# Performance work log

Measured on AMD Instinct MI355X. Metric: run time of the kernel, lower is better.

## Reference

```python
import jax, jax.numpy as jnp
import numpy as np
import math

B, H, S, DK = 2, 16, 2048, 64

def setup_inputs() -> dict:
    key = jax.random.key(0)
    kq, kk, kv, km = jax.random.split(key, 4)
    q = jax.random.normal(kq, (B, H, S, DK), dtype=jnp.float32)
    k = jax.random.normal(kk, (B, H, S, DK), dtype=jnp.float32)
    v = jax.random.normal(kv, (B, H, S, DK), dtype=jnp.float32)
    mask = jax.random.randint(km, (1, 1, S, S), 0, 2).astype(jnp.bool_)
    return {"q": q, "k": k, "v": v, "mask": mask}

def reference(q, k, v, mask):
    d_k = q.shape[-1]
    # scores: [B,H,Sq,Sk]
    scores = jnp.einsum('bhqd,bhkd->bhqk', q, k) / math.sqrt(d_k)
    scores = jnp.where(mask, jnp.float32(-1e9), scores)
    # NOTE: original uses nn.Softmax(dim=2) -> softmax over the QUERY axis
    attn = jax.nn.softmax(scores, axis=2)
    out = jnp.einsum('bhqk,bhkd->bhqd', attn, v)
    return out
```

## Files before the change

### kernel.cpp

```cpp
#include <hip/hip_runtime.h>
#include <math.h>

#define S_LEN 2048
#define NCH   32
#define N_BH  32

typedef short bf16x8 __attribute__((ext_vector_type(8)));
typedef _Float16 f16x8 __attribute__((ext_vector_type(8)));
typedef float f32x4  __attribute__((ext_vector_type(4)));
typedef unsigned short u16;
typedef unsigned short u16x8 __attribute__((ext_vector_type(8)));
typedef unsigned long long u64;

#define MFMA32(a,b,c) __builtin_amdgcn_mfma_f32_16x16x32_bf16((a),(b),(c),0,0,0)
#define MFMAH(a,b,c)  __builtin_amdgcn_mfma_f32_16x16x32_f16((a),(b),(c),0,0,0)
#define EXP2(x) __builtin_amdgcn_exp2f(x)

#define SC        0.18033688011112042f
#define MASKED_L2 (-14.0f)

__device__ __forceinline__ u16 f2h(float x) {
  union { _Float16 h; u16 u; } v;
  v.h = (_Float16)x;
  return v.u;
}
__device__ __forceinline__ u16 f2bf_rne(float x) {
  unsigned u = __float_as_uint(x);
  return (u16)((u + 0x7FFF + ((u >> 16) & 1)) >> 16);
}
__device__ __forceinline__ void bfsplit(float x, u16& h, u16& l) {
  unsigned u = __float_as_uint(x);
  h = (u16)(u >> 16);
  float hf = __uint_as_float(u & 0xFFFF0000u);
  l = f2bf_rne(x - hf);
}

__global__ __launch_bounds__(256) void pack_mask(
    const int* __restrict__ mask, u64* __restrict__ bits) {
  const int word = blockIdx.x * 4 + (threadIdx.x >> 6);
  const int lane = threadIdx.x & 63;
  const int row = word >> 5, wc = word & 31;
  int m = mask[(size_t)row * S_LEN + wc * 64 + lane];
  u64 b = __ballot(m != 0);
  if (lane == 0) bits[word] = b;
}

__global__ __launch_bounds__(256) void prep_qk(
    const float* __restrict__ Q, const float* __restrict__ K,
    u16* __restrict__ qf, u16* __restrict__ kf) {
  const int tid = threadIdx.x;
  const int slot = tid & 15, r0 = tid >> 4;
  const size_t rowbase = (size_t)blockIdx.x * 64;
#pragma unroll
  for (int p = 0; p < 4; ++p) {
    const size_t row = rowbase + p * 16 + r0;
    const size_t dst = row * 64 + ((slot * 4) ^ (((int)row & 7) << 3));
    float4 xq = *(const float4*)(Q + row * 64 + slot * 4);
    *(ushort4*)(qf + dst) = make_ushort4(
        f2h(xq.x * SC), f2h(xq.y * SC), f2h(xq.z * SC), f2h(xq.w * SC));
    float4 xk = *(const float4*)(K + row * 64 + slot * 4);
    *(ushort4*)(kf + dst) = make_ushort4(
        f2h(xk.x), f2h(xk.y), f2h(xk.z), f2h(xk.w));
  }
}

__global__ __launch_bounds__(256) void prep_w(
    const float* __restrict__ V, const float* __restrict__ part,
    u16* __restrict__ w_t) {
  __shared__ __align__(16) u16 ts[4096];
  const int tid = threadIdx.x;
  const int kc = blockIdx.x, bh = blockIdx.y;
  const int k = tid >> 2, dblk = (tid & 3) * 16;
  const size_t ko = (size_t)bh * S_LEN + kc * 64 + k;
  const float lsum = part[ko] + part[65536 + ko]
                   + part[131072 + ko] + part[196608 + ko];
  const float ilk = 1.0f / lsum;
  const float* vb = V + ko * 64 + dblk;
#pragma unroll
  for (int u = 0; u < 4; ++u) {
    float4 x = *(const float4*)(vb + u * 4);
    float xs[4] = {x.x, x.y, x.z, x.w};
#pragma unroll
    for (int e = 0; e < 4; ++e) {
      const int d = dblk + u * 4 + e;
      ts[d * 64 + (k ^ ((d & 7) << 3))] = f2h(xs[e] * ilk);
    }
  }
  __syncthreads();
  u16* dst = w_t + ((size_t)bh * NCH + kc) * 4096;
#pragma unroll
  for (int j = 0; j < 2; ++j)
    *(u16x8*)(dst + j * 2048 + tid * 8) = *(const u16x8*)(ts + j * 2048 + tid * 8);
}

__global__ __launch_bounds__(512, 4) void passA(
    const u16* __restrict__ qf, const u16* __restrict__ kf,
    const u64* __restrict__ mbits, float* __restrict__ part) {
  __shared__ __align__(16) u16 qbuf[4096];

  const int tid = threadIdx.x;
  const int lane = tid & 63;
  const int w = tid >> 6;
  const int c = lane & 15;
  const int g = lane >> 4;
  const int bx = blockIdx.x;
  const int bh = blockIdx.y;
  const int qp = blockIdx.z;

  const size_t bh_off = (size_t)bh * S_LEN * 64;
  const int swc = (c & 7) << 3;

  f16x8 ka[2][2];
#pragma unroll
  for (int t = 0; t < 2; ++t) {
    const int row = bx * 256 + w * 32 + t * 16 + c;
#pragma unroll
    for (int h = 0; h < 2; ++h)
      ka[t][h] = *(const f16x8*)(kf + bh_off + (size_t)row * 64
                                 + ((h * 32 + g * 8) ^ swc));
  }

  u16x8 stg = *(const u16x8*)(qf + bh_off + (size_t)(qp * 512) * 64 + tid * 8);

  float lp[2][4] = {{0.f, 0.f, 0.f, 0.f}, {0.f, 0.f, 0.f, 0.f}};
  const int word = bx * 4 + (w >> 1);
  const int sh0 = (w & 1) * 32;

  for (int qs = 0; qs < 8; ++qs) {
    __syncthreads();
    *(u16x8*)(qbuf + tid * 8) = stg;
    __syncthreads();
    if (qs + 1 < 8)
      stg = *(const u16x8*)(qf + bh_off
            + (size_t)(qp * 512 + (qs + 1) * 64) * 64 + tid * 8);

#pragma unroll
    for (int sub = 0; sub < 4; ++sub) {
      f16x8 fh[2];
      const int rb = sub * 1024 + c * 64;
#pragma unroll
      for (int h = 0; h < 2; ++h)
        fh[h] = *(const f16x8*)(qbuf + rb + ((h * 32 + g * 8) ^ swc));
      const int qrow = qp * 512 + qs * 64 + sub * 16 + c;
      const u64 mw = mbits[(size_t)qrow * NCH + word];
#pragma unroll
      for (int t = 0; t < 2; ++t) {
        f32x4 acc = {0.f, 0.f, 0.f, 0.f};
        acc = MFMAH(ka[t][0], fh[0], acc);
        acc = MFMAH(ka[t][1], fh[1], acc);
        const unsigned nib = (unsigned)(mw >> (sh0 + t * 16 + g * 4)) & 0xFu;
#pragma unroll
        for (int r = 0; r < 4; ++r) {
          const float s = ((nib >> r) & 1) ? MASKED_L2 : acc[r];
          lp[t][r] += EXP2(s);
        }
      }
    }
  }

#pragma unroll
  for (int off = 1; off < 16; off <<= 1)
#pragma unroll
    for (int t = 0; t < 2; ++t)
#pragma unroll
      for (int r = 0; r < 4; ++r) lp[t][r] += __shfl_xor(lp[t][r], off, 64);
  if (c == 0) {
#pragma unroll
    for (int t = 0; t < 2; ++t) {
      float4 o = {lp[t][0], lp[t][1], lp[t][2], lp[t][3]};
      *(float4*)(part + (size_t)qp * 65536 + (size_t)bh * S_LEN
                 + bx * 256 + w * 32 + t * 16 + g * 4) = o;
    }
  }
}

__global__ __launch_bounds__(256, 4) void passC(
    const u16* __restrict__ qf, const u16* __restrict__ kf,
    const u16* __restrict__ w_t, const u64* __restrict__ mbits,
    float* __restrict__ out) {
  __shared__ __align__(16) u16 sbuf[2][8192];
  __shared__ __align__(16) u16 p_s[4096];

  const int tid = threadIdx.x;
  const int lane = tid & 63;
  const int w = tid >> 6;
  const int c = lane & 15;
  const int g = lane >> 4;
  const int qc = blockIdx.x;
  const int bh = blockIdx.y;

  const size_t bh_off = (size_t)bh * S_LEN * 64;
  const u16* tb_k = kf + bh_off;
  const u16* tb_w = w_t + (size_t)bh * NCH * 4096;
  const int swc = (c & 7) << 3;

  const int qrow = qc * 64 + w * 16 + c;
  f16x8 qb_[2];
#pragma unroll
  for (int h = 0; h < 2; ++h)
    qb_[h] = *(const f16x8*)(qf + bh_off + (size_t)qrow * 64
                             + ((h * 32 + g * 8) ^ swc));

  f32x4 oacc[4];
#pragma unroll
  for (int dt = 0; dt < 4; ++dt) oacc[dt] = (f32x4){0.f, 0.f, 0.f, 0.f};

  const int pbase = w * 1024 + c * 64;
  const int so = tid * 8;

  u16x8 stg[4];
#pragma unroll
  for (int j = 0; j < 2; ++j) {
    stg[0 + j] = *(const u16x8*)(tb_k + j * 2048 + so);
    stg[2 + j] = *(const u16x8*)(tb_w + j * 2048 + so);
  }
#pragma unroll
  for (int j = 0; j < 2; ++j) {
    *(u16x8*)(&sbuf[0][0] + j * 2048 + so) = stg[0 + j];
    *(u16x8*)(&sbuf[0][0] + 4096 + j * 2048 + so) = stg[2 + j];
  }
  __syncthreads();

  int cur = 0;
  for (int kc = 0; kc < NCH; ++kc) {
    if (kc + 1 < NCH) {
      const size_t nb = (size_t)(kc + 1) * 4096;
#pragma unroll
      for (int j = 0; j < 2; ++j) {
        stg[0 + j] = *(const u16x8*)(tb_k + nb + j * 2048 + so);
        stg[2 + j] = *(const u16x8*)(tb_w + nb + j * 2048 + so);
      }
    }

    const u16* bufc = &sbuf[cur][0];
    const u64 mw = mbits[(size_t)qrow * NCH + kc];

#pragma unroll
    for (int kt = 0; kt < 4; ++kt) {
      const int kbase = (16 * kt + c) * 64;
      f16x8 ak0 = *(const f16x8*)(bufc + kbase + ((g * 8) ^ swc));
      f16x8 ak1 = *(const f16x8*)(bufc + kbase + ((32 + g * 8) ^ swc));
      f32x4 acc = {0.f, 0.f, 0.f, 0.f};
      acc = MFMAH(ak0, qb_[0], acc);
      acc = MFMAH(ak1, qb_[1], acc);
      const unsigned nib = (unsigned)(mw >> (kt * 16 + g * 4)) & 0xFu;
      u16 pb[4];
#pragma unroll
      for (int r = 0; r < 4; ++r) {
        const float s = ((nib >> r) & 1) ? MASKED_L2 : acc[r];
        pb[r] = f2h(EXP2(s));
      }
      *(ushort4*)(p_s + pbase + ((kt * 16 + g * 4) ^ swc)) =
          make_ushort4(pb[0], pb[1], pb[2], pb[3]);
    }

#pragma unroll
    for (int s2 = 0; s2 < 2; ++s2) {
      const int koff = (s2 * 32 + g * 8) ^ swc;
      f16x8 pb8 = *(const f16x8*)(p_s + pbase + koff);
#pragma unroll
      for (int dt = 0; dt < 4; ++dt) {
        f16x8 av = *(const f16x8*)(bufc + 4096 + (16 * dt + c) * 64 + koff);
        oacc[dt] = MFMAH(av, pb8, oacc[dt]);
      }
    }

    if (kc + 1 < NCH) {
      u16* bufn = &sbuf[cur ^ 1][0];
#pragma unroll
      for (int j = 0; j < 2; ++j) {
        *(u16x8*)(bufn + j * 2048 + so) = stg[0 + j];
        *(u16x8*)(bufn + 4096 + j * 2048 + so) = stg[2 + j];
      }
    }
    __syncthreads();
    cur ^= 1;
  }

  float* ob = out + (bh_off + (size_t)qrow * 64);
#pragma unroll
  for (int dt = 0; dt < 4; ++dt) {
    float4 o = {oacc[dt][0], oacc[dt][1], oacc[dt][2], oacc[dt][3]};
    *(float4*)(ob + dt * 16 + g * 4) = o;
  }
}

__global__ __launch_bounds__(256) void passA_colsum(
    const float* __restrict__ Q, const float* __restrict__ K,
    const u64* __restrict__ mbits, float* __restrict__ il_out) {
  const int tid = threadIdx.x;
  const int lane = tid & 63;
  const int w = tid >> 6;
  const int c = lane & 15;
  const int g = lane >> 4;
  const int kc = blockIdx.x;
  const int bh = blockIdx.y;

  const float* Qb = Q + (size_t)bh * S_LEN * 64;
  const float* Kb = K + (size_t)bh * S_LEN * 64;

  bf16x8 kah[2], kal[2];
  {
    const int krow = kc * 64 + w * 16 + c;
#pragma unroll
    for (int h = 0; h < 2; ++h) {
      const float* src = Kb + (size_t)krow * 64 + h * 32 + g * 8;
      float4 x = *(const float4*)(src);
      float4 y = *(const float4*)(src + 4);
      float xs[8] = {x.x, x.y, x.z, x.w, y.x, y.y, y.z, y.w};
#pragma unroll
      for (int e = 0; e < 8; ++e) {
        u16 hh, ll; bfsplit(xs[e], hh, ll);
        kah[h][e] = (short)hh; kal[h][e] = (short)ll;
      }
    }
  }

  float lp[4] = {0.f, 0.f, 0.f, 0.f};
  const int shift = w * 16 + g * 4;

  for (int qs = 0; qs < S_LEN / 16; ++qs) {
    const int qrow = qs * 16 + c;
    bf16x8 qbh_[2], qbl_[2];
#pragma unroll
    for (int h = 0; h < 2; ++h) {
      const float* src = Qb + (size_t)qrow * 64 + h * 32 + g * 8;
      float4 x = *(const float4*)(src);
      float4 y = *(const float4*)(src + 4);
      float xs[8] = {x.x, x.y, x.z, x.w, y.x, y.y, y.z, y.w};
#pragma unroll
      for (int e = 0; e < 8; ++e) {
        u16 hh, ll; bfsplit(xs[e] * SC, hh, ll);
        qbh_[h][e] = (short)hh; qbl_[h][e] = (short)ll;
      }
    }
    f32x4 acc = {0.f, 0.f, 0.f, 0.f};
#pragma unroll
    for (int h = 0; h < 2; ++h) {
      acc = MFMA32(kah[h], qbh_[h], acc);
      acc = MFMA32(kal[h], qbh_[h], acc);
      acc = MFMA32(kah[h], qbl_[h], acc);
    }
    u64 mw = mbits[(size_t)qrow * NCH + kc];
    unsigned nib = (unsigned)(mw >> shift) & 0xFu;
#pragma unroll
    for (int r = 0; r < 4; ++r) {
      float s = ((nib >> r) & 1) ? -30.0f : acc[r];
      lp[r] += exp2f(s);
    }
  }
#pragma unroll
  for (int off = 1; off < 16; off <<= 1)
#pragma unroll
    for (int r = 0; r < 4; ++r) lp[r] += __shfl_xor(lp[r], off, 64);
  if (c == 0) {
    float4 o = {1.f / lp[0], 1.f / lp[1], 1.f / lp[2], 1.f / lp[3]};
    *(float4*)(il_out + (size_t)bh * S_LEN + kc * 64 + w * 16 + g * 4) = o;
  }
}

__global__ __launch_bounds__(256) void passC_out(
    const float* __restrict__ Q, const float* __restrict__ K,
    const float* __restrict__ V, const u64* __restrict__ mbits,
    const float* __restrict__ il_in, float* __restrict__ out) {
  __shared__ u16 kh_s[4096];
  __shared__ u16 kl_s[4096];
  __shared__ u16 vt_s[4096];
  __shared__ u16 p_s[4096];

  const int tid = threadIdx.x;
  const int lane = tid & 63;
  const int w = tid >> 6;
  const int c = lane & 15;
  const int g = lane >> 4;
  const int qc = blockIdx.x;
  const int bh = blockIdx.y;

  const float* Qb = Q + (size_t)bh * S_LEN * 64;
  const float* Kb = K + (size_t)bh * S_LEN * 64;
  const float* Vb = V + (size_t)bh * S_LEN * 64;

  bf16x8 qbh_[2], qbl_[2];
  {
    const int qrow = qc * 64 + w * 16 + c;
#pragma unroll
    for (int h = 0; h < 2; ++h) {
      const float* src = Qb + (size_t)qrow * 64 + h * 32 + g * 8;
      float4 x = *(const float4*)(src);
      float4 y = *(const float4*)(src + 4);
      float xs[8] = {x.x, x.y, x.z, x.w, y.x, y.y, y.z, y.w};
#pragma unroll
      for (int e = 0; e < 8; ++e) {
        u16 hh, ll; bfsplit(xs[e] * SC, hh, ll);
        qbh_[h][e] = (short)hh; qbl_[h][e] = (short)ll;
      }
    }
  }

  f32x4 oacc[4];
#pragma unroll
  for (int dt = 0; dt < 4; ++dt) oacc[dt] = (f32x4){0.f, 0.f, 0.f, 0.f};

  const int slot = tid & 15, r0 = tid >> 4;
  const int kv = tid & 63, dblk = tid >> 6;
  const int swc = (c & 7) << 3;
  const int pbase = w * 1024 + c * 64;

  for (int kc = 0; kc < NCH; ++kc) {
    __syncthreads();
#pragma unroll
    for (int p = 0; p < 4; ++p) {
      const int row = p * 16 + r0;
      float4 kx = *(const float4*)(Kb + (size_t)(kc * 64 + row) * 64 + slot * 4);
      float xs[4] = {kx.x, kx.y, kx.z, kx.w};
      u16 ha[4], la[4];
#pragma unroll
      for (int e = 0; e < 4; ++e) bfsplit(xs[e], ha[e], la[e]);
      const int idx = row * 64 + ((slot * 4) ^ ((row & 7) << 3));
      *(ushort4*)(kh_s + idx) = make_ushort4(ha[0], ha[1], ha[2], ha[3]);
      *(ushort4*)(kl_s + idx) = make_ushort4(la[0], la[1], la[2], la[3]);
    }
    {
      const float ilk = il_in[(size_t)bh * S_LEN + kc * 64 + kv];
#pragma unroll
      for (int u = 0; u < 4; ++u) {
        float4 vv = *(const float4*)(Vb + (size_t)(kc * 64 + kv) * 64 + dblk * 16 + u * 4);
        float xs[4] = {vv.x, vv.y, vv.z, vv.w};
#pragma unroll
        for (int e = 0; e < 4; ++e) {
          const int d = dblk * 16 + u * 4 + e;
          vt_s[d * 64 + (kv ^ ((d & 7) << 3))] = f2bf_rne(xs[e] * ilk);
        }
      }
    }
    __syncthreads();

    const u64 mw = mbits[(size_t)(qc * 64 + w * 16 + c) * NCH + kc];

#pragma unroll
    for (int kt = 0; kt < 4; ++kt) {
      const int kbase = (16 * kt + c) * 64;
      bf16x8 akh[2], akl[2];
#pragma unroll
      for (int h = 0; h < 2; ++h) {
        const int off = (h * 32 + g * 8) ^ swc;
        akh[h] = *(const bf16x8*)(kh_s + kbase + off);
        akl[h] = *(const bf16x8*)(kl_s + kbase + off);
      }
      f32x4 acc = {0.f, 0.f, 0.f, 0.f};
#pragma unroll
      for (int h = 0; h < 2; ++h) {
        acc = MFMA32(akh[h], qbh_[h], acc);
        acc = MFMA32(akl[h], qbh_[h], acc);
        acc = MFMA32(akh[h], qbl_[h], acc);
      }
      const unsigned nib = (unsigned)(mw >> (kt * 16 + g * 4)) & 0xFu;
      u16 pb[4];
#pragma unroll
      for (int r = 0; r < 4; ++r) {
        const float s = ((nib >> r) & 1) ? -30.0f : acc[r];
        pb[r] = f2bf_rne(exp2f(s));
      }
      *(ushort4*)(p_s + pbase + ((kt * 16 + g * 4) ^ swc)) =
          make_ushort4(pb[0], pb[1], pb[2], pb[3]);
    }
    __syncthreads();

#pragma unroll
    for (int s = 0; s < 2; ++s) {
      const int koff = (s * 32 + 8 * g) ^ swc;
      bf16x8 pb8 = *(const bf16x8*)(p_s + pbase + koff);
#pragma unroll
      for (int dt = 0; dt < 4; ++dt) {
        bf16x8 av = *(const bf16x8*)(vt_s + (16 * dt + c) * 64 + koff);
        oacc[dt] = MFMA32(av, pb8, oacc[dt]);
      }
    }
  }

  float* ob = out + ((size_t)bh * S_LEN + qc * 64 + w * 16 + c) * 64;
#pragma unroll
  for (int dt = 0; dt < 4; ++dt) {
    float4 o = {oacc[dt][0], oacc[dt][1], oacc[dt][2], oacc[dt][3]};
    *(float4*)(ob + dt * 16 + g * 4) = o;
  }
}

extern "C" void kernel_launch(void* const* d_in, const int* in_sizes, int n_in,
                              void* d_out, int out_size, void* d_ws, size_t ws_size,
                              hipStream_t stream) {
  (void)in_sizes; (void)n_in; (void)out_size;
  const float* q = (const float*)d_in[0];
  const float* k = (const float*)d_in[1];
  const float* v = (const float*)d_in[2];
  const int* mask = (const int*)d_in[3];
  float* out = (float*)d_out;

  u64* mbits = (u64*)d_ws;
  float* part = (float*)((char*)d_ws + 524288);
  const size_t PL = (size_t)N_BH * S_LEN * 64;
  u16* qf = (u16*)((char*)d_ws + 524288 + 1048576);
  u16* kf = qf + PL;
  u16* w_t = kf + PL;
  const size_t need = 524288 + 1048576 + 3 * PL * sizeof(u16);

  pack_mask<<<dim3(S_LEN * NCH / 4), 256, 0, stream>>>(mask, mbits);

  if (ws_size >= need) {
    prep_qk<<<dim3(1024), 256, 0, stream>>>(q, k, qf, kf);
    passA<<<dim3(8, N_BH, 4), 512, 0, stream>>>(qf, kf, mbits, part);
    prep_w<<<dim3(NCH, N_BH), 256, 0, stream>>>(v, part, w_t);
    passC<<<dim3(NCH, N_BH), 256, 0, stream>>>(qf, kf, w_t, mbits, out);
  } else {
    float* il = part;
    dim3 grid(NCH, N_BH);
    passA_colsum<<<grid, 256, 0, stream>>>(q, k, mbits, il);
    passC_out<<<grid, 256, 0, stream>>>(q, k, v, mbits, il, out);
  }
}
```

Measured before the change: 126.3 us.

## Fuse mask packing into prep kernel, double-buffer passA Q tile, add MFMA priority

```diff
diff --git a/kernel.cpp b/kernel.cpp
--- a/kernel.cpp
+++ b/kernel.cpp
@@ -7,6 +7,7 @@
 
 typedef short bf16x8 __attribute__((ext_vector_type(8)));
 typedef _Float16 f16x8 __attribute__((ext_vector_type(8)));
+typedef __fp16 fp16x2 __attribute__((ext_vector_type(2)));
 typedef float f32x4  __attribute__((ext_vector_type(4)));
 typedef unsigned short u16;
 typedef unsigned short u16x8 __attribute__((ext_vector_type(8)));
@@ -17,7 +18,7 @@
 #define EXP2(x) __builtin_amdgcn_exp2f(x)
 
 #define SC        0.18033688011112042f
-#define MASKED_L2 (-14.0f)
+#define MASKED_P  6.103515625e-05f
 
 __device__ __forceinline__ u16 f2h(float x) {
   union { _Float16 h; u16 u; } v;
@@ -45,22 +46,33 @@
   if (lane == 0) bits[word] = b;
 }
 
-__global__ __launch_bounds__(256) void prep_qk(
+__global__ __launch_bounds__(256) void prep_qk_mask(
     const float* __restrict__ Q, const float* __restrict__ K,
-    u16* __restrict__ qf, u16* __restrict__ kf) {
+    const int* __restrict__ mask,
+    u16* __restrict__ qf, u16* __restrict__ kf, u64* __restrict__ bits) {
+  const int b = blockIdx.x;
   const int tid = threadIdx.x;
-  const int slot = tid & 15, r0 = tid >> 4;
-  const size_t rowbase = (size_t)blockIdx.x * 64;
-#pragma unroll
-  for (int p = 0; p < 4; ++p) {
-    const size_t row = rowbase + p * 16 + r0;
-    const size_t dst = row * 64 + ((slot * 4) ^ (((int)row & 7) << 3));
-    float4 xq = *(const float4*)(Q + row * 64 + slot * 4);
-    *(ushort4*)(qf + dst) = make_ushort4(
-        f2h(xq.x * SC), f2h(xq.y * SC), f2h(xq.z * SC), f2h(xq.w * SC));
-    float4 xk = *(const float4*)(K + row * 64 + slot * 4);
-    *(ushort4*)(kf + dst) = make_ushort4(
-        f2h(xk.x), f2h(xk.y), f2h(xk.z), f2h(xk.w));
+  if (b < 1024) {
+    const int slot = tid & 15, r0 = tid >> 4;
+    const size_t rowbase = (size_t)b * 64;
+#pragma unroll
+    for (int p = 0; p < 4; ++p) {
+      const size_t row = rowbase + p * 16 + r0;
+      const size_t dst = row * 64 + ((slot * 4) ^ (((int)row & 7) << 3));
+      float4 xq = *(const float4*)(Q + row * 64 + slot * 4);
+      *(ushort4*)(qf + dst) = make_ushort4(
+          f2h(xq.x * SC), f2h(xq.y * SC), f2h(xq.z * SC), f2h(xq.w * SC));
+      float4 xk = *(const float4*)(K + row * 64 + slot * 4);
+      *(ushort4*)(kf + dst) = make_ushort4(
+          f2h(xk.x), f2h(xk.y), f2h(xk.z), f2h(xk.w));
+    }
+  } else {
+    const int word = (b - 1024) * 4 + (tid >> 6);
+    const int lane = tid & 63;
+    const int row = word >> 5, wc = word & 31;
+    int m = mask[(size_t)row * S_LEN + wc * 64 + lane];
+    u64 bb = __ballot(m != 0);
+    if (lane == 0) bits[word] = bb;
   }
 }
 
@@ -96,7 +108,7 @@
 __global__ __launch_bounds__(512, 4) void passA(
     const u16* __restrict__ qf, const u16* __restrict__ kf,
     const u64* __restrict__ mbits, float* __restrict__ part) {
-  __shared__ __align__(16) u16 qbuf[4096];
+  __shared__ __align__(16) u16 qbuf[2][4096];
 
   const int tid = threadIdx.x;
   const int lane = tid & 63;
@@ -121,41 +133,49 @@
   }
 
   u16x8 stg = *(const u16x8*)(qf + bh_off + (size_t)(qp * 512) * 64 + tid * 8);
+  *(u16x8*)(&qbuf[0][0] + tid * 8) = stg;
+  __syncthreads();
 
   float lp[2][4] = {{0.f, 0.f, 0.f, 0.f}, {0.f, 0.f, 0.f, 0.f}};
   const int word = bx * 4 + (w >> 1);
   const int sh0 = (w & 1) * 32;
 
+  int cur = 0;
   for (int qs = 0; qs < 8; ++qs) {
-    __syncthreads();
-    *(u16x8*)(qbuf + tid * 8) = stg;
-    __syncthreads();
     if (qs + 1 < 8)
       stg = *(const u16x8*)(qf + bh_off
             + (size_t)(qp * 512 + (qs + 1) * 64) * 64 + tid * 8);
 
+    const u16* qb = &qbuf[cur][0];
 #pragma unroll
     for (int sub = 0; sub < 4; ++sub) {
       f16x8 fh[2];
       const int rb = sub * 1024 + c * 64;
 #pragma unroll
       for (int h = 0; h < 2; ++h)
-        fh[h] = *(const f16x8*)(qbuf + rb + ((h * 32 + g * 8) ^ swc));
+        fh[h] = *(const f16x8*)(qb + rb + ((h * 32 + g * 8) ^ swc));
       const int qrow = qp * 512 + qs * 64 + sub * 16 + c;
       const u64 mw = mbits[(size_t)qrow * NCH + word];
 #pragma unroll
       for (int t = 0; t < 2; ++t) {
         f32x4 acc = {0.f, 0.f, 0.f, 0.f};
+        __builtin_amdgcn_s_setprio(1);
         acc = MFMAH(ka[t][0], fh[0], acc);
         acc = MFMAH(ka[t][1], fh[1], acc);
+        __builtin_amdgcn_s_setprio(0);
         const unsigned nib = (unsigned)(mw >> (sh0 + t * 16 + g * 4)) & 0xFu;
 #pragma unroll
         for (int r = 0; r < 4; ++r) {
-          const float s = ((nib >> r) & 1) ? MASKED_L2 : acc[r];
-          lp[t][r] += EXP2(s);
+          const float tv = EXP2(acc[r]);
+          lp[t][r] += ((nib >> r) & 1) ? MASKED_P : tv;
         }
       }
     }
+
+    if (qs + 1 < 8)
+      *(u16x8*)(&qbuf[cur ^ 1][0] + tid * 8) = stg;
+    __syncthreads();
+    cur ^= 1;
   }
 
 #pragma unroll
@@ -241,19 +261,24 @@
       f16x8 ak0 = *(const f16x8*)(bufc + kbase + ((g * 8) ^ swc));
       f16x8 ak1 = *(const f16x8*)(bufc + kbase + ((32 + g * 8) ^ swc));
       f32x4 acc = {0.f, 0.f, 0.f, 0.f};
+      __builtin_amdgcn_s_setprio(1);
       acc = MFMAH(ak0, qb_[0], acc);
       acc = MFMAH(ak1, qb_[1], acc);
+      __builtin_amdgcn_s_setprio(0);
       const unsigned nib = (unsigned)(mw >> (kt * 16 + g * 4)) & 0xFu;
-      u16 pb[4];
+      float p[4];
 #pragma unroll
       for (int r = 0; r < 4; ++r) {
-        const float s = ((nib >> r) & 1) ? MASKED_L2 : acc[r];
-        pb[r] = f2h(EXP2(s));
-      }
-      *(ushort4*)(p_s + pbase + ((kt * 16 + g * 4) ^ swc)) =
-          make_ushort4(pb[0], pb[1], pb[2], pb[3]);
-    }
-
+        const float tv = EXP2(acc[r]);
+        p[r] = ((nib >> r) & 1) ? MASKED_P : tv;
+      }
+      union { fp16x2 h; unsigned u; } cl, ch;
+      cl.h = __builtin_amdgcn_cvt_pkrtz(p[0], p[1]);
+      ch.h = __builtin_amdgcn_cvt_pkrtz(p[2], p[3]);
+      *(uint2*)(p_s + pbase + ((kt * 16 + g * 4) ^ swc)) = make_uint2(cl.u, ch.u);
+    }
+
+    __builtin_amdgcn_s_setprio(1);
 #pragma unroll
     for (int s2 = 0; s2 < 2; ++s2) {
       const int koff = (s2 * 32 + g * 8) ^ swc;
@@ -264,6 +289,7 @@
         oacc[dt] = MFMAH(av, pb8, oacc[dt]);
       }
     }
+    __builtin_amdgcn_s_setprio(0);
 
     if (kc + 1 < NCH) {
       u16* bufn = &sbuf[cur ^ 1][0];
@@ -504,14 +530,14 @@
   u16* w_t = kf + PL;
   const size_t need = 524288 + 1048576 + 3 * PL * sizeof(u16);
 
-  pack_mask<<<dim3(S_LEN * NCH / 4), 256, 0, stream>>>(mask, mbits);
-
   if (ws_size >= need) {
-    prep_qk<<<dim3(1024), 256, 0, stream>>>(q, k, qf, kf);
+    prep_qk_mask<<<dim3(1024 + S_LEN * NCH / 4), 256, 0, stream>>>(
+        q, k, mask, qf, kf, mbits);
     passA<<<dim3(8, N_BH, 4), 512, 0, stream>>>(qf, kf, mbits, part);
     prep_w<<<dim3(NCH, N_BH), 256, 0, stream>>>(v, part, w_t);
     passC<<<dim3(NCH, N_BH), 256, 0, stream>>>(qf, kf, w_t, mbits, out);
   } else {
+    pack_mask<<<dim3(S_LEN * NCH / 4), 256, 0, stream>>>(mask, mbits);
     float* il = part;
     dim3 grid(NCH, N_BH);
     passA_colsum<<<grid, 256, 0, stream>>>(q, k, mbits, il);
```

New measurement: 124.8 us. About the same (-1.2%).
